# Performance work log

Hardware: AMD Instinct MI355X
Metric: run time of the kernel (lower is better)

The kernel has to match this reference:

```python
import jax, jax.numpy as jnp
import numpy as np

D_MODEL = 2048
N_HEADS = 16
D_HEAD = D_MODEL // N_HEADS
BATCH = 2
SEQ = 2048
NEG = -1e9


def setup_inputs() -> dict:
    key = jax.random.key(0)
    ks = jax.random.split(key, 6)
    s = 1.0 / np.sqrt(D_MODEL)
    x = jax.random.normal(ks[0], (BATCH, SEQ, D_MODEL), dtype=jnp.float32)
    # additive causal mask: 0 on/below diagonal, -1e9 above
    causal = jnp.where(jnp.tril(jnp.ones((SEQ, SEQ), dtype=bool)), 0.0, NEG).astype(jnp.float32)
    return {
        "x": x,
        "mask": causal,
        "Wq": jax.random.normal(ks[1], (D_MODEL, D_MODEL), dtype=jnp.float32) * s,
        "bq": jnp.zeros((D_MODEL,), dtype=jnp.float32),
        "Wk": jax.random.normal(ks[2], (D_MODEL, D_MODEL), dtype=jnp.float32) * s,
        "bk": jnp.zeros((D_MODEL,), dtype=jnp.float32),
        "Wv": jax.random.normal(ks[3], (D_MODEL, D_MODEL), dtype=jnp.float32) * s,
        "bv": jnp.zeros((D_MODEL,), dtype=jnp.float32),
        "Wo": jax.random.normal(ks[4], (D_MODEL, D_MODEL), dtype=jnp.float32) * s,
        "bo": jnp.zeros((D_MODEL,), dtype=jnp.float32),
    }


def reference(x, mask, Wq, bq, Wk, bk, Wv, bv, Wo, bo):
    B, S, _ = x.shape
    scale = 1.0 / np.sqrt(D_HEAD).astype(np.float32)
    # projections -> (B, H, S, Dh)
    def split_heads(t):
        return t.reshape(B, S, N_HEADS, D_HEAD).transpose(0, 2, 1, 3)
    q = split_heads(x @ Wq + bq)
    k = split_heads(x @ Wk + bk)
    v = split_heads(x @ Wv + bv)
    scores = jnp.einsum("bhqd,bhkd->bhqk", q, k) * scale + mask  # (B,H,S,S)
    weights = jax.nn.softmax(scores, axis=-1)
    attn = jnp.einsum("bhqk,bhkd->bhqd", weights, v)
    attn = attn.transpose(0, 2, 1, 3).reshape(B, S, D_MODEL)
    return attn @ Wo + bo
```

## Files before the change

kernel.cpp:

```cpp
#include <hip/hip_runtime.h>
#include <hip/hip_bf16.h>
#include <math.h>

typedef __bf16 bf16;
typedef __attribute__((ext_vector_type(8))) __bf16 bf16x8;
typedef __attribute__((ext_vector_type(4))) float f32x4;
typedef __attribute__((ext_vector_type(4))) int i32x4;

#define DEV __device__ __forceinline__

static constexpr int S_LEN = 2048;
static constexpr int DM = 2048;
static constexpr int NB = 2;
static constexpr int NH = 16;
static constexpr int DH = 128;
static constexpr long MROWS = (long)NB * S_LEN;

static constexpr float QSCALE = 0.12751744836522312f;
static constexpr float M0 = 11.0f;


__global__ void k_cast_bf16(const float* __restrict__ in, bf16* __restrict__ out, long n8) {
  long i = (long)blockIdx.x * blockDim.x + threadIdx.x;
  long stride = (long)gridDim.x * blockDim.x;
  for (; i < n8; i += stride) {
    const float4* p = (const float4*)(in + i * 8);
    float4 a = p[0], b = p[1];
    bf16x8 v;
    v[0] = (bf16)a.x; v[1] = (bf16)a.y; v[2] = (bf16)a.z; v[3] = (bf16)a.w;
    v[4] = (bf16)b.x; v[5] = (bf16)b.y; v[6] = (bf16)b.z; v[7] = (bf16)b.w;
    *(bf16x8*)(out + i * 8) = v;
  }
}

__global__ void k_transpose_w(const float* __restrict__ in, bf16* __restrict__ out) {
  __shared__ float t[32][33];
  int bx = blockIdx.x * 32, by = blockIdx.y * 32;
  int tx = threadIdx.x, ty = threadIdx.y;
#pragma unroll
  for (int i = 0; i < 32; i += 8)
    t[ty + i][tx] = in[(long)(by + ty + i) * DM + bx + tx];
  __syncthreads();
#pragma unroll
  for (int i = 0; i < 32; i += 8)
    out[(long)(bx + ty + i) * DM + by + tx] = (bf16)t[tx][ty + i];
}

__global__ void k_transpose_v(const bf16* __restrict__ v, bf16* __restrict__ vt) {
  __shared__ bf16 t[32][33];
  int s0 = blockIdx.x * 32, d0 = blockIdx.y * 32;
  int bh = blockIdx.z;
  int b = bh >> 4, h = bh & 15;
  int tx = threadIdx.x, ty = threadIdx.y;
  const bf16* src = v + ((long)(b * S_LEN + s0)) * DM + h * DH + d0;
#pragma unroll
  for (int i = 0; i < 32; i += 8)
    t[ty + i][tx] = src[(long)(ty + i) * DM + tx];
  __syncthreads();
  bf16* dst = vt + ((long)bh * DH + d0) * S_LEN + s0;
#pragma unroll
  for (int i = 0; i < 32; i += 8)
    dst[(long)(ty + i) * S_LEN + tx] = t[tx][ty + i];
}


template<int ROWB>
DEV void stage16k(const bf16* __restrict__ g, long gstride, bf16* l, int tid) {
#pragma unroll
  for (int c = 0; c < 4; ++c) {
    int o = c * 4096 + tid * 16;
    int row = o / ROWB;
    int blk = (o & (ROWB - 1)) >> 4;
    int blkg = blk ^ (row & 7);
    const bf16* src = g + (long)row * gstride + (blkg << 3);
    char* dst = (char*)l + (o & ~1023);
    __builtin_amdgcn_global_load_lds(
        (const __attribute__((address_space(1))) void*)src,
        (__attribute__((address_space(3))) void*)dst, 16, 0, 0);
  }
}

DEV void stage_k(const bf16* __restrict__ g, bf16* l, int tid) {
#pragma unroll
  for (int c = 0; c < 4; ++c) {
    int o = c * 4096 + tid * 16;
    int row = o >> 8;
    int blk = (o >> 4) & 15;
    int blkg = blk ^ (row & 7);
    int prow = (row & 3) | (((row >> 2) & 3) << 3) | (((row >> 5) & 1) << 2) |
               (((row >> 4) & 1) << 5);
    const bf16* src = g + (long)prow * DM + (blkg << 3);
    char* dst = (char*)l + (o & ~1023);
    __builtin_amdgcn_global_load_lds(
        (const __attribute__((address_space(1))) void*)src,
        (__attribute__((address_space(3))) void*)dst, 16, 0, 0);
  }
}

template<int ROWB>
DEV bf16x8 read_frag(const bf16* l, int row, int blk) {
  int blks = blk ^ (row & 7);
  return *(const bf16x8*)((const char*)l + row * ROWB + (blks << 4));
}


template<bool OUT_BF16>
__global__ __launch_bounds__(256) void k_gemm_bt(const bf16* __restrict__ A,
                                                 const bf16* __restrict__ BT,
                                                 const float* __restrict__ bias,
                                                 void* __restrict__ C,
                                                 int M, int N, int K, float cs) {
  __shared__ __align__(16) bf16 lA[128 * 64];
  __shared__ __align__(16) bf16 lB[128 * 64];
  int tid = threadIdx.x;
  int row0 = blockIdx.y * 128, col0 = blockIdx.x * 128;
  int w = tid >> 6, lane = tid & 63;
  int wm = w >> 1, wn = w & 1;
  int g = lane >> 4, c16 = lane & 15;

  f32x4 acc[4][4] = {};

  for (int kt = 0; kt < K; kt += 64) {
    stage16k<128>(A + (long)row0 * K + kt, K, lA, tid);
    stage16k<128>(BT + (long)col0 * K + kt, K, lB, tid);
    __syncthreads();
#pragma unroll
    for (int ks = 0; ks < 2; ++ks) {
      bf16x8 af[4], bf_[4];
#pragma unroll
      for (int i = 0; i < 4; ++i)
        af[i] = read_frag<128>(lA, wm * 64 + i * 16 + c16, ks * 4 + g);
#pragma unroll
      for (int j = 0; j < 4; ++j)
        bf_[j] = read_frag<128>(lB, wn * 64 + j * 16 + c16, ks * 4 + g);
#pragma unroll
      for (int i = 0; i < 4; ++i)
#pragma unroll
        for (int j = 0; j < 4; ++j)
          acc[i][j] = __builtin_amdgcn_mfma_f32_16x16x32_bf16(af[i], bf_[j], acc[i][j], 0, 0, 0);
    }
    __syncthreads();
  }

#pragma unroll
  for (int i = 0; i < 4; ++i) {
    int grow = row0 + wm * 64 + i * 16 + (g << 2);
#pragma unroll
    for (int j = 0; j < 4; ++j) {
      int gcol = col0 + wn * 64 + j * 16 + c16;
      float bv = bias[gcol];
#pragma unroll
      for (int r = 0; r < 4; ++r) {
        float vv = (acc[i][j][r] + bv) * cs;
        if constexpr (OUT_BF16)
          ((bf16*)C)[(long)(grow + r) * N + gcol] = (bf16)vv;
        else
          ((float*)C)[(long)(grow + r) * N + gcol] = vv;
      }
    }
  }
}


__global__ __launch_bounds__(256, 2) void k_attn(const bf16* __restrict__ Q,
                                                 const bf16* __restrict__ Kt,
                                                 const bf16* __restrict__ Vt,
                                                 bf16* __restrict__ O) {
  __shared__ __align__(16) bf16 sK[2][64 * 128];
  __shared__ __align__(16) bf16 sV[2][128 * 64];

  int tid = threadIdx.x;
  int bid = blockIdx.x;
  int bh = bid & 31;
  int u0 = bid >> 5;
  int qt = (u0 < 8) ? u0 : 23 - u0;
  int b = bh >> 4, h = bh & 15;
  int q0 = qt * 128;
  int nt = 2 * qt + 2;
  int w = tid >> 6, lane = tid & 63;
  int g = lane >> 4, c16 = lane & 15;
  int qb = q0 + w * 32;

  const bf16* Qh = Q + (long)b * S_LEN * DM + h * DH;
  const bf16* Kh = Kt + (long)b * S_LEN * DM + h * DH;
  const bf16* Vh = Vt + (long)bh * DH * S_LEN;

  bf16x8 qa[2][4];
#pragma unroll
  for (int u = 0; u < 2; ++u)
#pragma unroll
    for (int ks = 0; ks < 4; ++ks)
      qa[u][ks] = *(const bf16x8*)(Qh + (long)(qb + 16 * u + c16) * DM + (ks * 4 + g) * 8);

  stage_k(Kh, sK[0], tid);
  stage16k<128>(Vh, S_LEN, sV[0], tid);

  float lsum[2] = {0.f, 0.f};
  f32x4 od[2][8] = {};

#pragma unroll 1
  for (int kt = 0; kt < nt; ++kt) {
    int cur = kt & 1;
    if (kt + 1 < nt) {
      stage_k(Kh + (long)(kt + 1) * 64 * DM, sK[cur ^ 1], tid);
      stage16k<128>(Vh + (kt + 1) * 64, S_LEN, sV[cur ^ 1], tid);
      asm volatile("s_waitcnt vmcnt(8)" ::: "memory");
    } else {
      asm volatile("s_waitcnt vmcnt(0)" ::: "memory");
    }
    __builtin_amdgcn_s_barrier();
    asm volatile("" ::: "memory");

    int kv0 = kt * 64;
    if (kv0 <= qb + 31) {
      f32x4 sf[2][4] = {};
      __builtin_amdgcn_s_setprio(1);
#pragma unroll
      for (int n = 0; n < 4; ++n)
#pragma unroll
        for (int ks = 0; ks < 4; ++ks) {
          bf16x8 kf = read_frag<256>(sK[cur], n * 16 + c16, ks * 4 + g);
          sf[0][n] = __builtin_amdgcn_mfma_f32_16x16x32_bf16(kf, qa[0][ks], sf[0][n], 0, 0, 0);
          sf[1][n] = __builtin_amdgcn_mfma_f32_16x16x32_bf16(kf, qa[1][ks], sf[1][n], 0, 0, 0);
        }
      __builtin_amdgcn_s_setprio(0);

      bool emask = (kv0 + 63 > qb);
      bf16x8 pa[2][2];
#pragma unroll
      for (int u = 0; u < 2; ++u) {
        unsigned pw[8];
#pragma unroll
        for (int n = 0; n < 4; ++n) {
          float p[4];
#pragma unroll
          for (int r = 0; r < 4; ++r) {
            float s = sf[u][n][r];
            if (emask) {
              int kv = kv0 + ((n & 1) << 5) + (g << 3) + ((n >> 1) << 2) + r;
              int qg = qb + 16 * u + c16;
              s = (kv > qg) ? -INFINITY : s;
            }
            float pv = exp2f(s - M0);
            p[r] = pv;
            lsum[u] += pv;
          }
          asm("v_cvt_pk_bf16_f32 %0, %1, %2" : "=v"(pw[2 * n]) : "v"(p[0]), "v"(p[1]));
          asm("v_cvt_pk_bf16_f32 %0, %1, %2" : "=v"(pw[2 * n + 1]) : "v"(p[2]), "v"(p[3]));
        }
        i32x4 t0 = {(int)pw[0], (int)pw[1], (int)pw[4], (int)pw[5]};
        i32x4 t1 = {(int)pw[2], (int)pw[3], (int)pw[6], (int)pw[7]};
        pa[u][0] = __builtin_bit_cast(bf16x8, t0);
        pa[u][1] = __builtin_bit_cast(bf16x8, t1);
      }

      __builtin_amdgcn_s_setprio(1);
#pragma unroll
      for (int j = 0; j < 8; ++j)
#pragma unroll
        for (int ks = 0; ks < 2; ++ks) {
          bf16x8 vf = read_frag<128>(sV[cur], j * 16 + c16, ks * 4 + g);
          od[0][j] = __builtin_amdgcn_mfma_f32_16x16x32_bf16(pa[0][ks], vf, od[0][j], 0, 0, 0);
          od[1][j] = __builtin_amdgcn_mfma_f32_16x16x32_bf16(pa[1][ks], vf, od[1][j], 0, 0, 0);
        }
      __builtin_amdgcn_s_setprio(0);
    }
    asm volatile("" ::: "memory");
    __builtin_amdgcn_s_barrier();
  }

#pragma unroll
  for (int u = 0; u < 2; ++u) {
    lsum[u] += __shfl_xor(lsum[u], 16);
    lsum[u] += __shfl_xor(lsum[u], 32);
  }
  const long ob = ((long)(b * S_LEN + qb)) * DM + h * DH + c16;
#pragma unroll
  for (int u = 0; u < 2; ++u)
#pragma unroll
    for (int r = 0; r < 4; ++r) {
      float inv = 1.0f / __shfl(lsum[u], 4 * g + r);
#pragma unroll
      for (int j = 0; j < 8; ++j)
        O[ob + (long)(16 * u + 4 * g + r) * DM + j * 16] = (bf16)(od[u][j][r] * inv);
    }
}


extern "C" void kernel_launch(void* const* d_in, const int* in_sizes, int n_in,
                              void* d_out, int out_size, void* d_ws, size_t ws_size,
                              hipStream_t stream) {
  (void)in_sizes; (void)n_in; (void)out_size; (void)ws_size;
  const float* x  = (const float*)d_in[0];
  const float* Wq = (const float*)d_in[2];
  const float* bq = (const float*)d_in[3];
  const float* Wk = (const float*)d_in[4];
  const float* bk = (const float*)d_in[5];
  const float* Wv = (const float*)d_in[6];
  const float* bv = (const float*)d_in[7];
  const float* Wo = (const float*)d_in[8];
  const float* bo = (const float*)d_in[9];
  float* out = (float*)d_out;

  bf16* Xb = (bf16*)d_ws;
  bf16* WT = Xb + MROWS * DM;
  bf16* Qb = WT + (long)DM * DM;
  bf16* Kb = Qb + MROWS * DM;
  bf16* Vb = Kb + MROWS * DM;
  bf16* Vt = Xb;
  bf16* A2 = Vb;

  dim3 tb32(32, 8);
  dim3 gW(64, 64);
  dim3 gGemm(DM / 128, MROWS / 128);

  k_cast_bf16<<<2048, 256, 0, stream>>>(x, Xb, MROWS * DM / 8);

  k_transpose_w<<<gW, tb32, 0, stream>>>(Wq, WT);
  k_gemm_bt<true><<<gGemm, 256, 0, stream>>>(Xb, WT, bq, Qb, (int)MROWS, DM, DM, QSCALE);
  k_transpose_w<<<gW, tb32, 0, stream>>>(Wk, WT);
  k_gemm_bt<true><<<gGemm, 256, 0, stream>>>(Xb, WT, bk, Kb, (int)MROWS, DM, DM, 1.0f);
  k_transpose_w<<<gW, tb32, 0, stream>>>(Wv, WT);
  k_gemm_bt<true><<<gGemm, 256, 0, stream>>>(Xb, WT, bv, Vb, (int)MROWS, DM, DM, 1.0f);

  k_transpose_v<<<dim3(S_LEN / 32, DH / 32, NB * NH), tb32, 0, stream>>>(Vb, Vt);

  k_attn<<<512, 256, 0, stream>>>(Qb, Kb, Vt, A2);

  k_transpose_w<<<gW, tb32, 0, stream>>>(Wo, WT);
  k_gemm_bt<false><<<gGemm, 256, 0, stream>>>(A2, WT, bo, out, (int)MROWS, DM, DM, 1.0f);
}
```

Before: 295.3 us.

## Split long causal attention tiles across blocks and merge partial results

Attention work is rebalanced. Each role-0 block runs one short query tile in full, then the first part of a long query tile's KV range. Each role-1 block runs the rest of that long tile's KV range. Partial unnormalized outputs and row sums go to scratch space in the output buffer, and a new merge kernel adds them and normalizes. This removes tail imbalance from causal tiles of uneven length, at the cost of extra scratch traffic and one more kernel launch.

```diff
diff --git a/kernel.cpp b/kernel.cpp
--- a/kernel.cpp
+++ b/kernel.cpp
@@ -165,125 +165,181 @@
 __global__ __launch_bounds__(256, 2) void k_attn(const bf16* __restrict__ Q,
                                                  const bf16* __restrict__ Kt,
                                                  const bf16* __restrict__ Vt,
-                                                 bf16* __restrict__ O) {
+                                                 bf16* __restrict__ O,
+                                                 bf16* __restrict__ part,
+                                                 float* __restrict__ lsums) {
   __shared__ __align__(16) bf16 sK[2][64 * 128];
   __shared__ __align__(16) bf16 sV[2][128 * 64];
 
   int tid = threadIdx.x;
   int bid = blockIdx.x;
   int bh = bid & 31;
-  int u0 = bid >> 5;
-  int qt = (u0 < 8) ? u0 : 23 - u0;
+  int pr = (bid >> 5) & 7;
+  int role = bid >> 8;
   int b = bh >> 4, h = bh & 15;
-  int q0 = qt * 128;
-  int nt = 2 * qt + 2;
   int w = tid >> 6, lane = tid & 63;
   int g = lane >> 4, c16 = lane & 15;
-  int qb = q0 + w * 32;
+  int t = bh * 8 + pr;
 
   const bf16* Qh = Q + (long)b * S_LEN * DM + h * DH;
   const bf16* Kh = Kt + (long)b * S_LEN * DM + h * DH;
   const bf16* Vh = Vt + (long)bh * DH * S_LEN;
 
-  bf16x8 qa[2][4];
-#pragma unroll
-  for (int u = 0; u < 2; ++u)
-#pragma unroll
-    for (int ks = 0; ks < 4; ++ks)
-      qa[u][ks] = *(const bf16x8*)(Qh + (long)(qb + 16 * u + c16) * DM + (ks * 4 + g) * 8);
-
-  stage_k(Kh, sK[0], tid);
-  stage16k<128>(Vh, S_LEN, sV[0], tid);
-
-  float lsum[2] = {0.f, 0.f};
-  f32x4 od[2][8] = {};
-
 #pragma unroll 1
-  for (int kt = 0; kt < nt; ++kt) {
-    int cur = kt & 1;
-    if (kt + 1 < nt) {
-      stage_k(Kh + (long)(kt + 1) * 64 * DM, sK[cur ^ 1], tid);
-      stage16k<128>(Vh + (kt + 1) * 64, S_LEN, sV[cur ^ 1], tid);
-      asm volatile("s_waitcnt vmcnt(8)" ::: "memory");
+  for (int seg = 0; seg < 2; ++seg) {
+    int qt, k0, k1, partial;
+    if (role == 0) {
+      if (seg == 0) { qt = pr;      k0 = 0;           k1 = 2 * pr + 2;  partial = 0; }
+      else          { qt = 15 - pr; k0 = 0;           k1 = 15 - 2 * pr; partial = 1; }
     } else {
-      asm volatile("s_waitcnt vmcnt(0)" ::: "memory");
-    }
-    __builtin_amdgcn_s_barrier();
-    asm volatile("" ::: "memory");
-
-    int kv0 = kt * 64;
-    if (kv0 <= qb + 31) {
-      f32x4 sf[2][4] = {};
-      __builtin_amdgcn_s_setprio(1);
-#pragma unroll
-      for (int n = 0; n < 4; ++n)
-#pragma unroll
-        for (int ks = 0; ks < 4; ++ks) {
-          bf16x8 kf = read_frag<256>(sK[cur], n * 16 + c16, ks * 4 + g);
-          sf[0][n] = __builtin_amdgcn_mfma_f32_16x16x32_bf16(kf, qa[0][ks], sf[0][n], 0, 0, 0);
-          sf[1][n] = __builtin_amdgcn_mfma_f32_16x16x32_bf16(kf, qa[1][ks], sf[1][n], 0, 0, 0);
+      if (seg == 1) break;
+      qt = 15 - pr; k0 = 15 - 2 * pr; k1 = 32 - 2 * pr; partial = 2;
+    }
+
+    int q0 = qt * 128;
+    int qb = q0 + w * 32;
+
+    bf16x8 qa[2][4];
+#pragma unroll
+    for (int u = 0; u < 2; ++u)
+#pragma unroll
+      for (int ks = 0; ks < 4; ++ks)
+        qa[u][ks] = *(const bf16x8*)(Qh + (long)(qb + 16 * u + c16) * DM + (ks * 4 + g) * 8);
+
+    stage_k(Kh + (long)k0 * 64 * DM, sK[0], tid);
+    stage16k<128>(Vh + k0 * 64, S_LEN, sV[0], tid);
+
+    float lsum[2] = {0.f, 0.f};
+    f32x4 od[2][8] = {};
+
+#pragma unroll 1
+    for (int kt = k0; kt < k1; ++kt) {
+      int cur = (kt - k0) & 1;
+      if (kt + 1 < k1) {
+        stage_k(Kh + (long)(kt + 1) * 64 * DM, sK[cur ^ 1], tid);
+        stage16k<128>(Vh + (kt + 1) * 64, S_LEN, sV[cur ^ 1], tid);
+        asm volatile("s_waitcnt vmcnt(8)" ::: "memory");
+      } else {
+        asm volatile("s_waitcnt vmcnt(0)" ::: "memory");
+      }
+      __builtin_amdgcn_s_barrier();
+      asm volatile("" ::: "memory");
+
+      int kv0 = kt * 64;
+      if (kv0 <= qb + 31) {
+        f32x4 sf[2][4] = {};
+        __builtin_amdgcn_s_setprio(1);
+#pragma unroll
+        for (int n = 0; n < 4; ++n)
+#pragma unroll
+          for (int ks = 0; ks < 4; ++ks) {
+            bf16x8 kf = read_frag<256>(sK[cur], n * 16 + c16, ks * 4 + g);
+            sf[0][n] = __builtin_amdgcn_mfma_f32_16x16x32_bf16(kf, qa[0][ks], sf[0][n], 0, 0, 0);
+            sf[1][n] = __builtin_amdgcn_mfma_f32_16x16x32_bf16(kf, qa[1][ks], sf[1][n], 0, 0, 0);
+          }
+        __builtin_amdgcn_s_setprio(0);
+
+        bool emask = (kv0 + 63 > qb);
+        bf16x8 pa[2][2];
+#pragma unroll
+        for (int u = 0; u < 2; ++u) {
+          unsigned pw[8];
+#pragma unroll
+          for (int n = 0; n < 4; ++n) {
+            float p[4];
+#pragma unroll
+            for (int r = 0; r < 4; ++r) {
+              float s = sf[u][n][r];
+              if (emask) {
+                int kv = kv0 + ((n & 1) << 5) + (g << 3) + ((n >> 1) << 2) + r;
+                int qg = qb + 16 * u + c16;
+                s = (kv > qg) ? -INFINITY : s;
+              }
+              float pv = exp2f(s - M0);
+              p[r] = pv;
+              lsum[u] += pv;
+            }
+            asm("v_cvt_pk_bf16_f32 %0, %1, %2" : "=v"(pw[2 * n]) : "v"(p[0]), "v"(p[1]));
+            asm("v_cvt_pk_bf16_f32 %0, %1, %2" : "=v"(pw[2 * n + 1]) : "v"(p[2]), "v"(p[3]));
+          }
+          i32x4 t0 = {(int)pw[0], (int)pw[1], (int)pw[4], (int)pw[5]};
+          i32x4 t1 = {(int)pw[2], (int)pw[3], (int)pw[6], (int)pw[7]};
+          pa[u][0] = __builtin_bit_cast(bf16x8, t0);
+          pa[u][1] = __builtin_bit_cast(bf16x8, t1);
         }
-      __builtin_amdgcn_s_setprio(0);
-
-      bool emask = (kv0 + 63 > qb);
-      bf16x8 pa[2][2];
+
+        __builtin_amdgcn_s_setprio(1);
+#pragma unroll
+        for (int j = 0; j < 8; ++j)
+#pragma unroll
+          for (int ks = 0; ks < 2; ++ks) {
+            bf16x8 vf = read_frag<128>(sV[cur], j * 16 + c16, ks * 4 + g);
+            od[0][j] = __builtin_amdgcn_mfma_f32_16x16x32_bf16(pa[0][ks], vf, od[0][j], 0, 0, 0);
+            od[1][j] = __builtin_amdgcn_mfma_f32_16x16x32_bf16(pa[1][ks], vf, od[1][j], 0, 0, 0);
+          }
+        __builtin_amdgcn_s_setprio(0);
+      }
+      asm volatile("" ::: "memory");
+      __builtin_amdgcn_s_barrier();
+    }
+
+#pragma unroll
+    for (int u = 0; u < 2; ++u) {
+      lsum[u] += __shfl_xor(lsum[u], 16);
+      lsum[u] += __shfl_xor(lsum[u], 32);
+    }
+
+    if (partial == 0) {
+      const long ob = ((long)(b * S_LEN + qb)) * DM + h * DH + c16;
+#pragma unroll
+      for (int u = 0; u < 2; ++u)
+#pragma unroll
+        for (int r = 0; r < 4; ++r) {
+          float inv = 1.0f / __shfl(lsum[u], 4 * g + r);
+#pragma unroll
+          for (int j = 0; j < 8; ++j)
+            O[ob + (long)(16 * u + 4 * g + r) * DM + j * 16] = (bf16)(od[u][j][r] * inv);
+        }
+    } else {
+      bf16* PP = part + ((long)((partial == 2 ? 256 : 0) + t)) * 16384;
+      float* LP = lsums + (partial == 2 ? 256 * 128 : 0) + t * 128;
 #pragma unroll
       for (int u = 0; u < 2; ++u) {
-        unsigned pw[8];
-#pragma unroll
-        for (int n = 0; n < 4; ++n) {
-          float p[4];
-#pragma unroll
-          for (int r = 0; r < 4; ++r) {
-            float s = sf[u][n][r];
-            if (emask) {
-              int kv = kv0 + ((n & 1) << 5) + (g << 3) + ((n >> 1) << 2) + r;
-              int qg = qb + 16 * u + c16;
-              s = (kv > qg) ? -INFINITY : s;
-            }
-            float pv = exp2f(s - M0);
-            p[r] = pv;
-            lsum[u] += pv;
-          }
-          asm("v_cvt_pk_bf16_f32 %0, %1, %2" : "=v"(pw[2 * n]) : "v"(p[0]), "v"(p[1]));
-          asm("v_cvt_pk_bf16_f32 %0, %1, %2" : "=v"(pw[2 * n + 1]) : "v"(p[2]), "v"(p[3]));
+        if (g == 0) LP[32 * w + 16 * u + c16] = lsum[u];
+#pragma unroll
+        for (int r = 0; r < 4; ++r) {
+          int row = 32 * w + 16 * u + 4 * g + r;
+#pragma unroll
+          for (int j = 0; j < 8; ++j)
+            PP[row * 128 + 16 * j + c16] = (bf16)od[u][j][r];
         }
-        i32x4 t0 = {(int)pw[0], (int)pw[1], (int)pw[4], (int)pw[5]};
-        i32x4 t1 = {(int)pw[2], (int)pw[3], (int)pw[6], (int)pw[7]};
-        pa[u][0] = __builtin_bit_cast(bf16x8, t0);
-        pa[u][1] = __builtin_bit_cast(bf16x8, t1);
       }
-
-      __builtin_amdgcn_s_setprio(1);
-#pragma unroll
-      for (int j = 0; j < 8; ++j)
-#pragma unroll
-        for (int ks = 0; ks < 2; ++ks) {
-          bf16x8 vf = read_frag<128>(sV[cur], j * 16 + c16, ks * 4 + g);
-          od[0][j] = __builtin_amdgcn_mfma_f32_16x16x32_bf16(pa[0][ks], vf, od[0][j], 0, 0, 0);
-          od[1][j] = __builtin_amdgcn_mfma_f32_16x16x32_bf16(pa[1][ks], vf, od[1][j], 0, 0, 0);
-        }
-      __builtin_amdgcn_s_setprio(0);
-    }
-    asm volatile("" ::: "memory");
-    __builtin_amdgcn_s_barrier();
-  }
-
-#pragma unroll
-  for (int u = 0; u < 2; ++u) {
-    lsum[u] += __shfl_xor(lsum[u], 16);
-    lsum[u] += __shfl_xor(lsum[u], 32);
-  }
-  const long ob = ((long)(b * S_LEN + qb)) * DM + h * DH + c16;
-#pragma unroll
-  for (int u = 0; u < 2; ++u)
-#pragma unroll
-    for (int r = 0; r < 4; ++r) {
-      float inv = 1.0f / __shfl(lsum[u], 4 * g + r);
-#pragma unroll
-      for (int j = 0; j < 8; ++j)
-        O[ob + (long)(16 * u + 4 * g + r) * DM + j * 16] = (bf16)(od[u][j][r] * inv);
-    }
+    }
+  }
+}
+
+__global__ __launch_bounds__(256) void k_merge(const bf16* __restrict__ part,
+                                               const float* __restrict__ lsums,
+                                               bf16* __restrict__ A2) {
+  int t = blockIdx.x;
+  int bh = t >> 3, pr = t & 7;
+  int b = bh >> 4, h = bh & 15;
+  int qt = 15 - pr;
+  int tid = threadIdx.x;
+  int q = tid >> 1, d0 = (tid & 1) * 64;
+  float inv = 1.0f / (lsums[t * 128 + q] + lsums[256 * 128 + t * 128 + q]);
+  const bf16* pA = part + (long)t * 16384 + q * 128 + d0;
+  const bf16* pB = part + (long)(256 + t) * 16384 + q * 128 + d0;
+  bf16* out = A2 + ((long)(b * S_LEN + qt * 128 + q)) * DM + h * DH + d0;
+#pragma unroll
+  for (int j = 0; j < 8; ++j) {
+    bf16x8 a = *(const bf16x8*)(pA + j * 8);
+    bf16x8 bb = *(const bf16x8*)(pB + j * 8);
+    bf16x8 o;
+#pragma unroll
+    for (int r = 0; r < 8; ++r) o[r] = (bf16)(((float)a[r] + (float)bb[r]) * inv);
+    *(bf16x8*)(out + j * 8) = o;
+  }
 }
 
 
@@ -310,6 +366,9 @@
   bf16* Vt = Xb;
   bf16* A2 = Vb;
 
+  bf16* part = (bf16*)d_out;
+  float* lsums = (float*)((bf16*)d_out + 2L * 256 * 16384);
+
   dim3 tb32(32, 8);
   dim3 gW(64, 64);
   dim3 gGemm(DM / 128, MROWS / 128);
@@ -325,7 +384,8 @@
 
   k_transpose_v<<<dim3(S_LEN / 32, DH / 32, NB * NH), tb32, 0, stream>>>(Vb, Vt);
 
-  k_attn<<<512, 256, 0, stream>>>(Qb, Kb, Vt, A2);
+  k_attn<<<512, 256, 0, stream>>>(Qb, Kb, Vt, A2, part, lsums);
+  k_merge<<<256, 256, 0, stream>>>(part, lsums, A2);
 
   k_transpose_w<<<gW, tb32, 0, stream>>>(Wo, WT);
   k_gemm_bt<false><<<gGemm, 256, 0, stream>>>(A2, WT, bo, out, (int)MROWS, DM, DM, 1.0f);
```

Measured after the change: 293.2 us. Within noise of the previous version (-0.7%).
